# Kernel optimization log

Measured on AMD Instinct MI355X. Metric: run time of the kernel, lower is better.

## Reference

```python
import jax, jax.numpy as jnp
import numpy as np

NHEAD = 16
NUM_GROUPS = 4
EXPERTS_PER_GROUP = 2
LN_EPS = 1e-5


def _layernorm(x, g, b):
    mu = jnp.mean(x, axis=-1, keepdims=True)
    var = jnp.mean(jnp.square(x - mu), axis=-1, keepdims=True)
    return (x - mu) * jax.lax.rsqrt(var + LN_EPS) * g + b


def _mha(x, wi, bi, wo, bo):
    # torch nn.MultiheadAttention (batch_first): qkv = x @ in_proj_w.T + in_proj_b
    B, S, D = x.shape
    hd = D // NHEAD
    qkv = x @ wi.T + bi                      # [B,S,3D]
    q, k, v = jnp.split(qkv, 3, axis=-1)
    def heads(t):
        return t.reshape(B, S, NHEAD, hd).transpose(0, 2, 1, 3)  # [B,H,S,hd]
    q, k, v = heads(q), heads(k), heads(v)
    scores = jnp.einsum('bhqd,bhkd->bhqk', q, k) / jnp.sqrt(jnp.asarray(hd, x.dtype))
    attn = jax.nn.softmax(scores, axis=-1)
    o = jnp.einsum('bhqk,bhkd->bhqd', attn, v)
    o = o.transpose(0, 2, 1, 3).reshape(B, S, D)
    return o @ wo.T + bo


def _hier_moe(x, w_group, b_group, w_expert, b_expert, w1, b1, w2, b2):
    # Two-level top-1 routing: group gate -> expert gate within chosen group.
    B, S, D = x.shape
    xt = x.reshape(B * S, D)                 # [T,D]
    T = xt.shape[0]
    E = NUM_GROUPS * EXPERTS_PER_GROUP

    gp = jax.nn.softmax(xt @ w_group + b_group, axis=-1)          # [T,G]
    g_idx = jnp.argmax(gp, axis=-1)                                # [T]
    g_prob = jnp.max(gp, axis=-1)                                  # [T]

    elog = jnp.einsum('td,gde->tge', xt, w_expert) + b_expert      # [T,G,Epg]
    ep = jax.nn.softmax(elog, axis=-1)
    ep_sel = jnp.take_along_axis(ep, g_idx[:, None, None], axis=1)[:, 0, :]  # [T,Epg]
    e_idx_local = jnp.argmax(ep_sel, axis=-1)                      # [T]
    e_prob = jnp.max(ep_sel, axis=-1)                              # [T]

    flat_e = g_idx * EXPERTS_PER_GROUP + e_idx_local               # [T]
    combine = jax.nn.one_hot(flat_e, E, dtype=xt.dtype) * (g_prob * e_prob)[:, None]  # [T,E]

    # Dense dispatch (reference): run every expert on all tokens, combine with one-hot weights.
    h = jax.nn.relu(jnp.einsum('td,edf->etf', xt, w1) + b1[:, None, :])   # [E,T,Fff]
    y = jnp.einsum('etf,efd->etd', h, w2) + b2[:, None, :]                # [E,T,D]
    out = jnp.einsum('te,etd->td', combine, y)                            # [T,D]
    return out.reshape(B, S, D)


def setup_inputs() -> dict:
    key = jax.random.key(0)
    ks = jax.random.split(key, 8)
    B, S, D, F = 2, 1024, 1024, 2048
    G, Epg = NUM_GROUPS, EXPERTS_PER_GROUP
    E = G * Epg
    sc = lambda fan: 1.0 / np.sqrt(fan)
    return {
        'x': jax.random.normal(ks[0], (B, S, D), jnp.float32),
        'in_proj_w': jax.random.normal(ks[1], (3 * D, D), jnp.float32) * sc(D),
        'in_proj_b': jnp.zeros((3 * D,), jnp.float32),
        'out_proj_w': jax.random.normal(ks[2], (D, D), jnp.float32) * sc(D),
        'out_proj_b': jnp.zeros((D,), jnp.float32),
        'ln1_g': jnp.ones((D,), jnp.float32),
        'ln1_b': jnp.zeros((D,), jnp.float32),
        'ln2_g': jnp.ones((D,), jnp.float32),
        'ln2_b': jnp.zeros((D,), jnp.float32),
        'w_group': jax.random.normal(ks[3], (D, G), jnp.float32) * sc(D),
        'b_group': jnp.zeros((G,), jnp.float32),
        'w_expert': jax.random.normal(ks[4], (G, D, Epg), jnp.float32) * sc(D),
        'b_expert': jnp.zeros((G, Epg), jnp.float32),
        'w1': jax.random.normal(ks[5], (E, D, F), jnp.float32) * sc(D),
        'b1': jnp.zeros((E, F), jnp.float32),
        'w2': jax.random.normal(ks[6], (E, F, D), jnp.float32) * sc(F),
        'b2': jnp.zeros((E, D), jnp.float32),
    }


def reference(x, in_proj_w, in_proj_b, out_proj_w, out_proj_b,
              ln1_g, ln1_b, ln2_g, ln2_b,
              w_group, b_group, w_expert, b_expert, w1, b1, w2, b2):
    # Dropout p=0.1 is identity in eval mode.
    attn_out = _mha(x, in_proj_w, in_proj_b, out_proj_w, out_proj_b)
    x = _layernorm(x + attn_out, ln1_g, ln1_b)
    moe_out = _hier_moe(x, w_group, b_group, w_expert, b_expert, w1, b1, w2, b2)
    x = _layernorm(x + moe_out, ln2_g, ln2_b)
    return x
```

## Files before the change

kernel.cpp:

```cpp
#include <hip/hip_runtime.h>
#include <hip/hip_bf16.h>

#define TT 2048
#define DD 1024
#define FF 2048
#define SS 1024
#define NHD 16
#define HDD 64
#define NG 4
#define EPG 2
#define NE 8

#define QSC 0.18033688011112042f

typedef __attribute__((ext_vector_type(8))) short bf16x8;
typedef __attribute__((ext_vector_type(4))) float f32x4;
typedef __attribute__((ext_vector_type(4))) unsigned short ush4;

__device__ __forceinline__ unsigned short f2bf(float x) {
    unsigned int u = __float_as_uint(x);
    u = (u + 0x7fffu + ((u >> 16) & 1u)) >> 16;
    return (unsigned short)u;
}
__device__ __forceinline__ float bf2f(unsigned short h) {
    return __uint_as_float((unsigned int)h << 16);
}

__device__ __forceinline__ float wave_sum(float s) {
#pragma unroll
    for (int off = 32; off > 0; off >>= 1) s += __shfl_xor(s, off);
    return s;
}

__device__ __forceinline__ void gl16(const void* g, void* l) {
    auto gp = reinterpret_cast<const unsigned int __attribute__((address_space(1)))*>(
        (unsigned long long)g);
    auto lp = reinterpret_cast<unsigned int __attribute__((address_space(3)))*>(
        (unsigned int)(unsigned long long)l);
    __builtin_amdgcn_global_load_lds(gp, lp, 16, 0, 0);
}

__global__ __launch_bounds__(256) void split_bf16_kernel(
    const float* __restrict__ in, unsigned short* __restrict__ hi,
    unsigned short* __restrict__ lo, int n4)
{
    const int i = blockIdx.x * 256 + threadIdx.x;
    if (i >= n4) return;
    const float4 v = ((const float4*)in)[i];
    float vv[4] = {v.x, v.y, v.z, v.w};
    ush4 h, l;
#pragma unroll
    for (int j = 0; j < 4; ++j) {
        const unsigned short hb = f2bf(vv[j]);
        ((unsigned short*)&h)[j] = hb;
        ((unsigned short*)&l)[j] = f2bf(vv[j] - bf2f(hb));
    }
    ((ush4*)hi)[i] = h;
    ((ush4*)lo)[i] = l;
}

__global__ __launch_bounds__(256, 3) void gemm_split_kernel(
    const unsigned short* __restrict__ Ah, const unsigned short* __restrict__ Al,
    const unsigned short* __restrict__ Bh, const unsigned short* __restrict__ Bl,
    const float* __restrict__ bias, const float* __restrict__ resid,
    float* __restrict__ C, unsigned short* __restrict__ Chi,
    unsigned short* __restrict__ Clo, int qscale_n, int M, int N, int K)
{
    __shared__ unsigned short sAh[128 * 64];
    __shared__ unsigned short sAl[128 * 64];
    __shared__ unsigned short sBh[64 * 64];
    __shared__ unsigned short sBl[64 * 64];
    const int tid = threadIdx.x;
    const int lane = tid & 63, wid = tid >> 6;
    const int l15 = lane & 15, lg = lane >> 4;
    const int n0 = blockIdx.x << 6, m0 = blockIdx.y << 7;
    const int kper = K / gridDim.z;
    const int kbeg = blockIdx.z * kper, kend = kbeg + kper;
    float* __restrict__ Cz = C ? (C + (size_t)blockIdx.z * M * N) : C;

    f32x4 acc[2][4];
#pragma unroll
    for (int mi = 0; mi < 2; ++mi)
#pragma unroll
        for (int ni = 0; ni < 4; ++ni) acc[mi][ni] = (f32x4){0.f, 0.f, 0.f, 0.f};

    for (int k0 = kbeg; k0 < kend; k0 += 64) {
#pragma unroll
        for (int r = 0; r < 4; ++r) {
            const int s = (r << 8) + tid;
            const int row = s >> 3;
            const int cs = (s & 7) ^ (row & 7);
            const int lb = (s & ~63) << 3;
            const size_t ga = (size_t)(m0 + row) * K + k0 + (cs << 3);
            gl16(Ah + ga, &sAh[lb]);
            gl16(Al + ga, &sAl[lb]);
        }
#pragma unroll
        for (int r = 0; r < 2; ++r) {
            const int s = (r << 8) + tid;
            const int row = s >> 3;
            const int cs = (s & 7) ^ (row & 7);
            const int lb = (s & ~63) << 3;
            const size_t gb = (size_t)(n0 + row) * K + k0 + (cs << 3);
            gl16(Bh + gb, &sBh[lb]);
            gl16(Bl + gb, &sBl[lb]);
        }
        __syncthreads();
#pragma unroll
        for (int ks = 0; ks < 2; ++ks) {
            bf16x8 ah[2], al[2], bh[4], bl[4];
            const int ac = (ks << 2) + lg;
#pragma unroll
            for (int i = 0; i < 2; ++i) {
                const int ar = (wid << 5) + (i << 4) + l15;
                const int pa = ((ar << 3) | (ac ^ (ar & 7))) << 3;
                ah[i] = *(const bf16x8*)&sAh[pa];
                al[i] = *(const bf16x8*)&sAl[pa];
            }
#pragma unroll
            for (int i = 0; i < 4; ++i) {
                const int br = (i << 4) + l15;
                const int pb = ((br << 3) | (ac ^ (br & 7))) << 3;
                bh[i] = *(const bf16x8*)&sBh[pb];
                bl[i] = *(const bf16x8*)&sBl[pb];
            }
#pragma unroll
            for (int mi = 0; mi < 2; ++mi)
#pragma unroll
                for (int ni = 0; ni < 4; ++ni) {
                    acc[mi][ni] = __builtin_amdgcn_mfma_f32_16x16x32_bf16(ah[mi], bh[ni], acc[mi][ni], 0, 0, 0);
                    acc[mi][ni] = __builtin_amdgcn_mfma_f32_16x16x32_bf16(ah[mi], bl[ni], acc[mi][ni], 0, 0, 0);
                    acc[mi][ni] = __builtin_amdgcn_mfma_f32_16x16x32_bf16(al[mi], bh[ni], acc[mi][ni], 0, 0, 0);
                }
        }
        __syncthreads();
    }
#pragma unroll
    for (int mi = 0; mi < 2; ++mi)
#pragma unroll
        for (int ni = 0; ni < 4; ++ni)
#pragma unroll
            for (int r2 = 0; r2 < 4; ++r2) {
                const int m = m0 + (wid << 5) + (mi << 4) + (lg << 2) + r2;
                const int n = n0 + (ni << 4) + l15;
                float v = acc[mi][ni][r2];
                if (bias) v += bias[n];
                if (resid) v += resid[(size_t)m * N + n];
                const size_t idx = (size_t)m * N + n;
                if (Chi) {
                    if (n < qscale_n) v *= QSC;
                    const unsigned short hb = f2bf(v);
                    Chi[idx] = hb;
                    Clo[idx] = f2bf(v - bf2f(hb));
                } else {
                    Cz[idx] = v;
                }
            }
}

__global__ __launch_bounds__(256) void vtrans_kernel(
    const unsigned short* __restrict__ src, unsigned short* __restrict__ dst)
{
    __shared__ unsigned short tile[64][65];
    const int bh = blockIdx.y, b = bh >> 4, h = bh & 15;
    const int s0 = blockIdx.x << 6;
    const int tid = threadIdx.x;
#pragma unroll
    for (int r = 0; r < 2; ++r) {
        const int sl = tid + (r << 8);
        const int rr = sl >> 3, c8 = (sl & 7) << 3;
        const bf16x8 v = *(const bf16x8*)(src + (size_t)(b * SS + s0 + rr) * 3072 + 2048 + h * HDD + c8);
#pragma unroll
        for (int j = 0; j < 8; ++j) tile[rr][c8 + j] = ((const unsigned short*)&v)[j];
    }
    __syncthreads();
#pragma unroll
    for (int r = 0; r < 2; ++r) {
        const int sl = tid + (r << 8);
        const int d = sl >> 3, s8 = (sl & 7) << 3;
        bf16x8 o;
#pragma unroll
        for (int j = 0; j < 8; ++j) ((unsigned short*)&o)[j] = tile[s8 + j][d];
        *(bf16x8*)(dst + (size_t)(bh * HDD + d) * SS + s0 + s8) = o;
    }
}

__global__ __launch_bounds__(256, 4) void attn_mfma_kernel(
    const unsigned short* __restrict__ qh, const unsigned short* __restrict__ ql,
    const unsigned short* __restrict__ vth, const unsigned short* __restrict__ vtl,
    float* __restrict__ opart, float* __restrict__ mpart, float* __restrict__ lpart)
{
    __shared__ unsigned short sKh[4096], sKl[4096];
    __shared__ unsigned short sVh[4096], sVl[4096];
    const int bh = blockIdx.y, b = bh >> 4, h = bh & 15;
    const int q0 = blockIdx.x << 6;
    const int z = blockIdx.z;
    const int tid = threadIdx.x, lane = tid & 63, w = tid >> 6;
    const int l15 = lane & 15, lg = lane >> 4;

#pragma unroll
    for (int r = 0; r < 2; ++r) {
        const int s = (r << 8) + tid;
        const int row = s >> 3;
        const int cs = (s & 7) ^ (row & 7);
        const int lb = (s & ~63) << 3;
        const size_t gq = (size_t)(b * SS + q0 + row) * 3072 + h * HDD + (cs << 3);
        gl16(qh + gq, &sKh[lb]);
        gl16(ql + gq, &sKl[lb]);
    }
    __syncthreads();
    bf16x8 qah[2], qal[2];
#pragma unroll
    for (int ks = 0; ks < 2; ++ks) {
        const int ar = (w << 4) + l15;
        const int ac = (ks << 2) + lg;
        const int pa = ((ar << 3) | (ac ^ (ar & 7))) << 3;
        qah[ks] = *(const bf16x8*)&sKh[pa];
        qal[ks] = *(const bf16x8*)&sKl[pa];
    }
    __syncthreads();

    f32x4 accO[4];
#pragma unroll
    for (int nt = 0; nt < 4; ++nt) accO[nt] = (f32x4){0.f, 0.f, 0.f, 0.f};
    float m_run = -3.0e38f, l_run = 0.f;

    const int kvbeg = z << 9;
    for (int kv0 = kvbeg; kv0 < kvbeg + 512; kv0 += 64) {
#pragma unroll
        for (int r = 0; r < 2; ++r) {
            const int s = (r << 8) + tid;
            const int row = s >> 3;
            const int cs = (s & 7) ^ (row & 7);
            const int lb = (s & ~63) << 3;
            const size_t gk = (size_t)(b * SS + kv0 + row) * 3072 + DD + h * HDD + (cs << 3);
            gl16(qh + gk, &sKh[lb]);
            gl16(ql + gk, &sKl[lb]);
            const size_t gv = (size_t)(bh * HDD + row) * SS + kv0 + (cs << 3);
            gl16(vth + gv, &sVh[lb]);
            gl16(vtl + gv, &sVl[lb]);
        }
        __syncthreads();

        f32x4 sacc[4];
#pragma unroll
        for (int i = 0; i < 4; ++i) sacc[i] = (f32x4){0.f, 0.f, 0.f, 0.f};
        __builtin_amdgcn_s_setprio(1);
#pragma unroll
        for (int ks = 0; ks < 2; ++ks) {
            const int ac = (ks << 2) + lg;
#pragma unroll
            for (int i = 0; i < 4; ++i) {
                const int br = (i << 4) + l15;
                const int pb = ((br << 3) | (ac ^ (br & 7))) << 3;
                const bf16x8 kbh = *(const bf16x8*)&sKh[pb];
                const bf16x8 kbl = *(const bf16x8*)&sKl[pb];
                sacc[i] = __builtin_amdgcn_mfma_f32_16x16x32_bf16(kbh, qah[ks], sacc[i], 0, 0, 0);
                sacc[i] = __builtin_amdgcn_mfma_f32_16x16x32_bf16(kbh, qal[ks], sacc[i], 0, 0, 0);
                sacc[i] = __builtin_amdgcn_mfma_f32_16x16x32_bf16(kbl, qah[ks], sacc[i], 0, 0, 0);
            }
        }
        __builtin_amdgcn_s_setprio(0);
        __syncthreads();

        float mx = sacc[0][0];
#pragma unroll
        for (int i = 0; i < 4; ++i)
#pragma unroll
            for (int r2 = 0; r2 < 4; ++r2) mx = fmaxf(mx, sacc[i][r2]);
        mx = fmaxf(mx, __shfl_xor(mx, 16));
        mx = fmaxf(mx, __shfl_xor(mx, 32));
        const float mn = fmaxf(m_run, mx);
        const float corr = exp2f(m_run - mn);
        m_run = mn;
        float ls = 0.f;
        const int qrow = (w << 4) | l15;
#pragma unroll
        for (int i = 0; i < 4; ++i) {
            ush4 hp, lp;
#pragma unroll
            for (int r2 = 0; r2 < 4; ++r2) {
                const float p = exp2f(sacc[i][r2] - mn);
                ls += p;
                const unsigned short hb = (unsigned short)(__float_as_uint(p) >> 16);
                hp[r2] = hb;
                lp[r2] = (unsigned short)(__float_as_uint(p - bf2f(hb)) >> 16);
            }
            const int kvb = (i << 4) + (lg << 2);
            const int idx = (qrow << 6) + (((kvb >> 3) ^ (qrow & 7)) << 3) + (kvb & 7);
            *(ush4*)&sKh[idx] = hp;
            *(ush4*)&sKl[idx] = lp;
        }
        ls += __shfl_xor(ls, 16);
        ls += __shfl_xor(ls, 32);
        l_run = l_run * corr + ls;
        float c4[4];
#pragma unroll
        for (int r2 = 0; r2 < 4; ++r2)
            c4[r2] = __shfl(corr, (lane & 48) | ((lg << 2) + r2));
#pragma unroll
        for (int nt = 0; nt < 4; ++nt)
#pragma unroll
            for (int r2 = 0; r2 < 4; ++r2) accO[nt][r2] *= c4[r2];

        __builtin_amdgcn_s_setprio(1);
#pragma unroll
        for (int ks = 0; ks < 2; ++ks) {
            const int qq = (w << 4) + l15;
            const int slot = (ks << 2) + lg;
            const int pidx = (qq << 6) + ((slot ^ (qq & 7)) << 3);
            const bf16x8 pah = *(const bf16x8*)&sKh[pidx];
            const bf16x8 pal = *(const bf16x8*)&sKl[pidx];
            const int ac = (ks << 2) + lg;
#pragma unroll
            for (int nt = 0; nt < 4; ++nt) {
                const int dr = (nt << 4) + l15;
                const int pv = ((dr << 3) | (ac ^ (dr & 7))) << 3;
                const bf16x8 vbh = *(const bf16x8*)&sVh[pv];
                const bf16x8 vbl = *(const bf16x8*)&sVl[pv];
                accO[nt] = __builtin_amdgcn_mfma_f32_16x16x32_bf16(pah, vbh, accO[nt], 0, 0, 0);
                accO[nt] = __builtin_amdgcn_mfma_f32_16x16x32_bf16(pah, vbl, accO[nt], 0, 0, 0);
                accO[nt] = __builtin_amdgcn_mfma_f32_16x16x32_bf16(pal, vbh, accO[nt], 0, 0, 0);
            }
        }
        __builtin_amdgcn_s_setprio(0);
        __syncthreads();
    }

#pragma unroll
    for (int nt = 0; nt < 4; ++nt)
#pragma unroll
        for (int r2 = 0; r2 < 4; ++r2) {
            const int qq = q0 + (w << 4) + (lg << 2) + r2;
            const int dd = h * HDD + (nt << 4) + l15;
            opart[((size_t)z * TT + b * SS + qq) * DD + dd] = accO[nt][r2];
        }
    if (lane < 16) {
        const int qq = q0 + (w << 4) + lane;
        const int idx = z * (32 * SS) + bh * SS + qq;
        mpart[idx] = m_run;
        lpart[idx] = l_run;
    }
}

__global__ __launch_bounds__(256) void attn_combine_kernel(
    const float* __restrict__ opart, const float* __restrict__ mpart,
    const float* __restrict__ lpart, unsigned short* __restrict__ ohi,
    unsigned short* __restrict__ olo)
{
    const int t = blockIdx.x;
    const int tid = threadIdx.x;
    const int b = t >> 10, q = t & 1023;
    const int d0 = tid << 2;
    const int bh = (b << 4) + (d0 >> 6);
    const int mi = bh * SS + q;
    const float m0 = mpart[mi], m1 = mpart[32 * SS + mi];
    const float l0 = lpart[mi], l1 = lpart[32 * SS + mi];
    const float m = fmaxf(m0, m1);
    const float e0 = exp2f(m0 - m), e1 = exp2f(m1 - m);
    const float inv = 1.0f / (l0 * e0 + l1 * e1);
    const float4 a = *(const float4*)(opart + (size_t)t * DD + d0);
    const float4 c = *(const float4*)(opart + (size_t)(TT + t) * DD + d0);
    const float vv[4] = { (a.x * e0 + c.x * e1) * inv, (a.y * e0 + c.y * e1) * inv,
                          (a.z * e0 + c.z * e1) * inv, (a.w * e0 + c.w * e1) * inv };
    ush4 hh, ll;
#pragma unroll
    for (int j = 0; j < 4; ++j) {
        const unsigned short hb = f2bf(vv[j]);
        hh[j] = hb;
        ll[j] = f2bf(vv[j] - bf2f(hb));
    }
    *(ush4*)(ohi + (size_t)t * DD + d0) = hh;
    *(ush4*)(olo + (size_t)t * DD + d0) = ll;
}

__global__ __launch_bounds__(256) void ln_kernel(
    const float* __restrict__ in, const float* __restrict__ gamma,
    const float* __restrict__ beta, float* __restrict__ outf)
{
    const int t = blockIdx.x;
    const int tid = threadIdx.x;
    __shared__ float red[8];
    const float4 v = ((const float4*)(in + (size_t)t * DD))[tid];
    float s = v.x + v.y + v.z + v.w;
    s = wave_sum(s);
    const int wid = tid >> 6, lane = tid & 63;
    if (lane == 0) red[wid] = s;
    __syncthreads();
    const float mu = (red[0] + red[1] + red[2] + red[3]) * (1.0f / DD);
    const float d0 = v.x - mu, d1 = v.y - mu, d2 = v.z - mu, d3 = v.w - mu;
    float q = d0 * d0 + d1 * d1 + d2 * d2 + d3 * d3;
    q = wave_sum(q);
    if (lane == 0) red[4 + wid] = q;
    __syncthreads();
    const float var = (red[4] + red[5] + red[6] + red[7]) * (1.0f / DD);
    const float rstd = 1.0f / sqrtf(var + 1e-5f);
    const float4 g4 = ((const float4*)gamma)[tid];
    const float4 b4 = ((const float4*)beta)[tid];
    float4 ov = { d0 * rstd * g4.x + b4.x, d1 * rstd * g4.y + b4.y,
                  d2 * rstd * g4.z + b4.z, d3 * rstd * g4.w + b4.w };
    ((float4*)(outf + (size_t)t * DD))[tid] = ov;
}

__global__ __launch_bounds__(256) void ln_route_kernel(
    const float* __restrict__ x, const float* __restrict__ p0,
    const float* __restrict__ p1, const float* __restrict__ bo,
    const float* __restrict__ gamma, const float* __restrict__ beta,
    float* __restrict__ outf, unsigned short* __restrict__ outb,
    const float* __restrict__ wg, const float* __restrict__ bg,
    const float* __restrict__ we, const float* __restrict__ be,
    int* __restrict__ eid, float* __restrict__ gate, int* __restrict__ counts)
{
    const int t = blockIdx.x;
    const int tid = threadIdx.x;
    __shared__ float red[8];
    __shared__ float red2[4][12];
    const float4 xv = ((const float4*)(x + (size_t)t * DD))[tid];
    const float4 a4 = ((const float4*)(p0 + (size_t)t * DD))[tid];
    const float4 c4v = ((const float4*)(p1 + (size_t)t * DD))[tid];
    const float4 bo4 = ((const float4*)bo)[tid];
    const float4 v = { xv.x + a4.x + c4v.x + bo4.x, xv.y + a4.y + c4v.y + bo4.y,
                       xv.z + a4.z + c4v.z + bo4.z, xv.w + a4.w + c4v.w + bo4.w };
    float s = v.x + v.y + v.z + v.w;
    s = wave_sum(s);
    const int wid = tid >> 6, lane = tid & 63;
    if (lane == 0) red[wid] = s;
    __syncthreads();
    const float mu = (red[0] + red[1] + red[2] + red[3]) * (1.0f / DD);
    const float d0 = v.x - mu, d1 = v.y - mu, d2 = v.z - mu, d3 = v.w - mu;
    float q = d0 * d0 + d1 * d1 + d2 * d2 + d3 * d3;
    q = wave_sum(q);
    if (lane == 0) red[4 + wid] = q;
    __syncthreads();
    const float var = (red[4] + red[5] + red[6] + red[7]) * (1.0f / DD);
    const float rstd = 1.0f / sqrtf(var + 1e-5f);
    const float4 g4 = ((const float4*)gamma)[tid];
    const float4 b4 = ((const float4*)beta)[tid];
    const float o0 = d0 * rstd * g4.x + b4.x;
    const float o1 = d1 * rstd * g4.y + b4.y;
    const float o2 = d2 * rstd * g4.z + b4.z;
    const float o3 = d3 * rstd * g4.w + b4.w;
    float4 ov = {o0, o1, o2, o3};
    ((float4*)(outf + (size_t)t * DD))[tid] = ov;
    ush4 wv = { f2bf(o0), f2bf(o1), f2bf(o2), f2bf(o3) };
    *(ush4*)(outb + (size_t)t * DD + (tid << 2)) = wv;

    float pz[12];
#pragma unroll
    for (int k = 0; k < 12; ++k) pz[k] = 0.f;
    const float xo[4] = {o0, o1, o2, o3};
#pragma unroll
    for (int j = 0; j < 4; ++j) {
        const int c = (tid << 2) + j;
        const float xvv = xo[j];
        const float4 wgv = *(const float4*)(wg + c * NG);
        pz[0] = fmaf(xvv, wgv.x, pz[0]);
        pz[1] = fmaf(xvv, wgv.y, pz[1]);
        pz[2] = fmaf(xvv, wgv.z, pz[2]);
        pz[3] = fmaf(xvv, wgv.w, pz[3]);
#pragma unroll
        for (int g = 0; g < NG; ++g) {
            const float2 wev = *(const float2*)(we + ((size_t)g * DD + c) * EPG);
            pz[4 + 2 * g]     = fmaf(xvv, wev.x, pz[4 + 2 * g]);
            pz[4 + 2 * g + 1] = fmaf(xvv, wev.y, pz[4 + 2 * g + 1]);
        }
    }
#pragma unroll
    for (int k = 0; k < 12; ++k) pz[k] = wave_sum(pz[k]);
    if (lane == 0) {
#pragma unroll
        for (int k = 0; k < 12; ++k) red2[wid][k] = pz[k];
    }
    __syncthreads();
    if (tid == 0) {
        float zs[12];
#pragma unroll
        for (int k = 0; k < 12; ++k)
            zs[k] = red2[0][k] + red2[1][k] + red2[2][k] + red2[3][k];
        float z[NG];
#pragma unroll
        for (int g = 0; g < NG; ++g) z[g] = zs[g] + bg[g];
        int gi = 0; float zb = z[0];
#pragma unroll
        for (int g = 1; g < NG; ++g) if (z[g] > zb) { zb = z[g]; gi = g; }
        float se = 0.f;
#pragma unroll
        for (int g = 0; g < NG; ++g) se += __expf(z[g] - zb);
        const float gprob = 1.0f / se;
        float e0 = 0.f, e1 = 0.f;
#pragma unroll
        for (int g = 0; g < NG; ++g) {
            if (g == gi) {
                e0 = zs[4 + 2 * g] + be[g * EPG + 0];
                e1 = zs[4 + 2 * g + 1] + be[g * EPG + 1];
            }
        }
        const int ei = (e1 > e0) ? 1 : 0;
        const float ehi = ei ? e1 : e0, elo = ei ? e0 : e1;
        const float eprob = 1.0f / (1.0f + __expf(elo - ehi));
        eid[t] = gi * EPG + ei;
        gate[t] = gprob * eprob;
        atomicAdd(&counts[gi * EPG + ei], 1);
    }
}

__global__ void zero_counts_kernel(int* __restrict__ counts) {
    if (threadIdx.x < NE) counts[threadIdx.x] = 0;
}

__global__ void offsets_kernel(const int* __restrict__ counts, int* __restrict__ offs,
                               int* __restrict__ cursor) {
    if (threadIdx.x == 0) {
        int run = 0;
        for (int e = 0; e < NE; ++e) { offs[e] = run; cursor[e] = run; run += counts[e]; }
        offs[NE] = run;
    }
}

__global__ __launch_bounds__(256) void scatter_kernel(const int* __restrict__ eid,
                                                      int* __restrict__ cursor,
                                                      int* __restrict__ perm) {
    const int t = blockIdx.x * 256 + threadIdx.x;
    const int slot = atomicAdd(&cursor[eid[t]], 1);
    perm[slot] = t;
}

__global__ __launch_bounds__(256) void transpose_bf16_kernel(
    const float* __restrict__ in, unsigned short* __restrict__ out, int R, int C)
{
    __shared__ float tile[32][33];
    const int c0 = blockIdx.x << 5, r0 = blockIdx.y << 5;
    const size_t bo = (size_t)blockIdx.z * R * C;
    const int tc = threadIdx.x & 31, tr8 = threadIdx.x >> 5;
#pragma unroll
    for (int p = 0; p < 4; ++p) {
        const int rr = tr8 + (p << 3);
        tile[rr][tc] = in[bo + (size_t)(r0 + rr) * C + c0 + tc];
    }
    __syncthreads();
#pragma unroll
    for (int p = 0; p < 4; ++p) {
        const int rr = tr8 + (p << 3);
        out[bo + (size_t)(c0 + rr) * R + r0 + tc] = f2bf(tile[tc][rr]);
    }
}

__global__ __launch_bounds__(256, 4) void moe_gemm1_kernel(
    const unsigned short* __restrict__ x1b, const unsigned short* __restrict__ w1t,
    const float* __restrict__ b1, const int* __restrict__ offs,
    const int* __restrict__ perm, unsigned short* __restrict__ hbuf)
{
    const int e = blockIdx.y >> 5, mt = blockIdx.y & 31;
    const int row0 = offs[e] + (mt << 6);
    const int rend = offs[e + 1];
    if (row0 >= rend) return;
    const int valid = min(rend - row0, 64);
    const int n0 = blockIdx.x << 6;
    __shared__ unsigned short sA[2][64 * 64];
    __shared__ unsigned short sB[2][64 * 64];
    const int tid = threadIdx.x;
    const int lane = tid & 63, w = tid >> 6;
    const int l15 = lane & 15, lg = lane >> 4;

    size_t abase[2], bbase[2];
    int lbs[2];
#pragma unroll
    for (int r = 0; r < 2; ++r) {
        const int s = (r << 8) + tid;
        const int row = s >> 3;
        const int cs = (s & 7) ^ (row & 7);
        lbs[r] = (s & ~63) << 3;
        const int tk = perm[min(row0 + row, rend - 1)];
        abase[r] = (size_t)tk * DD + (cs << 3);
        bbase[r] = ((size_t)e * FF + n0 + row) * DD + (cs << 3);
    }

    f32x4 acc[4];
#pragma unroll
    for (int nt = 0; nt < 4; ++nt) acc[nt] = (f32x4){0.f, 0.f, 0.f, 0.f};

#pragma unroll
    for (int r = 0; r < 2; ++r) {
        gl16(x1b + abase[r], &sA[0][lbs[r]]);
        gl16(w1t + bbase[r], &sB[0][lbs[r]]);
    }
    __syncthreads();
    int cur = 0;
    for (int k0 = 0; k0 < DD; k0 += 64) {
        const int nxt = k0 + 64;
        if (nxt < DD) {
#pragma unroll
            for (int r = 0; r < 2; ++r) {
                gl16(x1b + abase[r] + nxt, &sA[cur ^ 1][lbs[r]]);
                gl16(w1t + bbase[r] + nxt, &sB[cur ^ 1][lbs[r]]);
            }
        }
#pragma unroll
        for (int ks = 0; ks < 2; ++ks) {
            const int ac = (ks << 2) + lg;
            const int ar = (w << 4) + l15;
            const int pa = ((ar << 3) | (ac ^ (ar & 7))) << 3;
            const bf16x8 a = *(const bf16x8*)&sA[cur][pa];
#pragma unroll
            for (int nt = 0; nt < 4; ++nt) {
                const int br = (nt << 4) + l15;
                const int pb = ((br << 3) | (ac ^ (br & 7))) << 3;
                acc[nt] = __builtin_amdgcn_mfma_f32_16x16x32_bf16(
                    a, *(const bf16x8*)&sB[cur][pb], acc[nt], 0, 0, 0);
            }
        }
        __syncthreads();
        cur ^= 1;
    }

    const float* bias = b1 + e * FF + n0;
    const int mbase = (w << 4) + (lg << 2);
#pragma unroll
    for (int nt = 0; nt < 4; ++nt) {
        const int n = (nt << 4) + l15;
#pragma unroll
        for (int r2 = 0; r2 < 4; ++r2) {
            const int m = mbase + r2;
            if (m < valid) {
                float v = fmaxf(acc[nt][r2] + bias[n], 0.f);
                hbuf[(size_t)(row0 + m) * FF + n0 + n] = f2bf(v);
            }
        }
    }
}

__global__ __launch_bounds__(256, 4) void moe_gemm2_kernel(
    const unsigned short* __restrict__ hbuf, const unsigned short* __restrict__ w2t,
    const int* __restrict__ offs, float* __restrict__ p0, float* __restrict__ p1)
{
    const int e = blockIdx.y >> 5, mt = blockIdx.y & 31;
    const int row0 = offs[e] + (mt << 6);
    const int rend = offs[e + 1];
    if (row0 >= rend) return;
    const int valid = min(rend - row0, 64);
    const int n0 = blockIdx.x << 6;
    const int z = blockIdx.z;
    float* __restrict__ pbuf = z ? p1 : p0;
    __shared__ unsigned short sA[2][64 * 64];
    __shared__ unsigned short sB[2][64 * 64];
    const int tid = threadIdx.x;
    const int lane = tid & 63, w = tid >> 6;
    const int l15 = lane & 15, lg = lane >> 4;

    size_t abase[2], bbase[2];
    int lbs[2];
#pragma unroll
    for (int r = 0; r < 2; ++r) {
        const int s = (r << 8) + tid;
        const int row = s >> 3;
        const int cs = (s & 7) ^ (row & 7);
        lbs[r] = (s & ~63) << 3;
        abase[r] = (size_t)(row0 + row) * FF + (cs << 3);
        bbase[r] = ((size_t)e * DD + n0 + row) * FF + (cs << 3);
    }

    f32x4 acc[4];
#pragma unroll
    for (int nt = 0; nt < 4; ++nt) acc[nt] = (f32x4){0.f, 0.f, 0.f, 0.f};

    const int kbeg = z << 10, kend = kbeg + 1024;
#pragma unroll
    for (int r = 0; r < 2; ++r) {
        gl16(hbuf + abase[r] + kbeg, &sA[0][lbs[r]]);
        gl16(w2t + bbase[r] + kbeg, &sB[0][lbs[r]]);
    }
    __syncthreads();
    int cur = 0;
    for (int k0 = kbeg; k0 < kend; k0 += 64) {
        const int nxt = k0 + 64;
        if (nxt < kend) {
#pragma unroll
            for (int r = 0; r < 2; ++r) {
                gl16(hbuf + abase[r] + nxt, &sA[cur ^ 1][lbs[r]]);
                gl16(w2t + bbase[r] + nxt, &sB[cur ^ 1][lbs[r]]);
            }
        }
#pragma unroll
        for (int ks = 0; ks < 2; ++ks) {
            const int ac = (ks << 2) + lg;
            const int ar = (w << 4) + l15;
            const int pa = ((ar << 3) | (ac ^ (ar & 7))) << 3;
            const bf16x8 a = *(const bf16x8*)&sA[cur][pa];
#pragma unroll
            for (int nt = 0; nt < 4; ++nt) {
                const int br = (nt << 4) + l15;
                const int pb = ((br << 3) | (ac ^ (br & 7))) << 3;
                acc[nt] = __builtin_amdgcn_mfma_f32_16x16x32_bf16(
                    a, *(const bf16x8*)&sB[cur][pb], acc[nt], 0, 0, 0);
            }
        }
        __syncthreads();
        cur ^= 1;
    }

    const int mbase = (w << 4) + (lg << 2);
#pragma unroll
    for (int nt = 0; nt < 4; ++nt) {
        const int n = (nt << 4) + l15;
#pragma unroll
        for (int r2 = 0; r2 < 4; ++r2) {
            const int m = mbase + r2;
            if (m < valid) pbuf[(size_t)(row0 + m) * DD + n0 + n] = acc[nt][r2];
        }
    }
}

__global__ __launch_bounds__(256) void moe2_combine_kernel(
    const float* __restrict__ p0, const float* __restrict__ p1,
    const int* __restrict__ offs, const int* __restrict__ perm,
    const float* __restrict__ gate, const float* __restrict__ b2,
    const float* __restrict__ x1, float* __restrict__ res2)
{
    const int s = blockIdx.x;
    const int tid = threadIdx.x;
    int e = 0;
#pragma unroll
    for (int g = 1; g < NE; ++g) e += (s >= offs[g]) ? 1 : 0;
    const int tk = perm[s];
    const float gt = gate[tk];
    const int c0 = tid << 2;
    const float4 a  = *(const float4*)(p0 + (size_t)s * DD + c0);
    const float4 b  = *(const float4*)(p1 + (size_t)s * DD + c0);
    const float4 bb = *(const float4*)(b2 + (size_t)e * DD + c0);
    const float4 xx = *(const float4*)(x1 + (size_t)tk * DD + c0);
    float4 o = { xx.x + gt * (a.x + b.x + bb.x), xx.y + gt * (a.y + b.y + bb.y),
                 xx.z + gt * (a.z + b.z + bb.z), xx.w + gt * (a.w + b.w + bb.w) };
    *(float4*)(res2 + (size_t)tk * DD + c0) = o;
}

extern "C" void kernel_launch(void* const* d_in, const int* in_sizes, int n_in,
                              void* d_out, int out_size, void* d_ws, size_t ws_size,
                              hipStream_t stream)
{
    (void)in_sizes; (void)n_in; (void)out_size; (void)ws_size;
    const float* x   = (const float*)d_in[0];
    const float* wi  = (const float*)d_in[1];
    const float* bi  = (const float*)d_in[2];
    const float* wo  = (const float*)d_in[3];
    const float* bo  = (const float*)d_in[4];
    const float* g1  = (const float*)d_in[5];
    const float* be1 = (const float*)d_in[6];
    const float* g2  = (const float*)d_in[7];
    const float* be2 = (const float*)d_in[8];
    const float* wgr = (const float*)d_in[9];
    const float* bgr = (const float*)d_in[10];
    const float* wex = (const float*)d_in[11];
    const float* bex = (const float*)d_in[12];
    const float* w1  = (const float*)d_in[13];
    const float* b1  = (const float*)d_in[14];
    const float* w2  = (const float*)d_in[15];
    const float* b2  = (const float*)d_in[16];
    float* out = (float*)d_out;

    char* ws = (char*)d_ws;
    unsigned short* qkvh  = (unsigned short*)(ws + 0);
    unsigned short* qkvl  = (unsigned short*)(ws + 12582912);
    unsigned short* hbuf  = (unsigned short*)(ws + 0);
    float* res2           = (float*)(ws + 8388608);
    unsigned short* vth   = (unsigned short*)(ws + 25165824);
    unsigned short* vtl   = (unsigned short*)(ws + 29360128);
    float* x1             = (float*)(ws + 41943040);
    unsigned short* x1b   = (unsigned short*)(ws + 50331648);
    unsigned short* w1t   = (unsigned short*)(ws + 54525952);
    unsigned short* w2t   = (unsigned short*)(ws + 88080384);
    char* misc = ws + 121634816;
    int*   eid    = (int*)(misc);
    float* gate   = (float*)(misc + 8192);
    int*   perm   = (int*)(misc + 16384);
    int*   counts = (int*)(misc + 24576);
    int*   offs   = (int*)(misc + 24640);
    int*   cursor = (int*)(misc + 24704);

    unsigned short* xs_hi = (unsigned short*)(ws + 33554432);
    unsigned short* xs_lo = (unsigned short*)(ws + 33554432 + 4194304);
    unsigned short* wi_hi = (unsigned short*)(ws + 54525952);
    unsigned short* wi_lo = (unsigned short*)(ws + 54525952 + 6291456);
    unsigned short* o_hi  = (unsigned short*)(ws + 41943040);
    unsigned short* o_lo  = (unsigned short*)(ws + 41943040 + 4194304);
    unsigned short* wo_hi = (unsigned short*)(ws + 88080384);
    unsigned short* wo_lo = (unsigned short*)(ws + 88080384 + 2097152);

    float* opart = (float*)(ws + 54525952);
    float* mpart = (float*)(ws + 54525952 + 16777216);
    float* lpart = (float*)(ws + 54525952 + 17039360);

    float* oproj = (float*)(ws + 0);

    float* mp0 = (float*)(ws + 16777216);
    float* mp1 = (float*)(ws + 25165824);

    zero_counts_kernel<<<dim3(1), dim3(64), 0, stream>>>(counts);

    split_bf16_kernel<<<dim3((TT * DD / 4 + 255) / 256), dim3(256), 0, stream>>>(x, xs_hi, xs_lo, TT * DD / 4);
    split_bf16_kernel<<<dim3((3 * DD * DD / 4 + 255) / 256), dim3(256), 0, stream>>>(wi, wi_hi, wi_lo, 3 * DD * DD / 4);
    gemm_split_kernel<<<dim3(3 * DD / 64, TT / 128, 1), dim3(256), 0, stream>>>(
        xs_hi, xs_lo, wi_hi, wi_lo, bi, (const float*)nullptr,
        (float*)nullptr, qkvh, qkvl, DD, TT, 3 * DD, DD);

    vtrans_kernel<<<dim3(SS / 64, 2 * NHD), dim3(256), 0, stream>>>(qkvh, vth);
    vtrans_kernel<<<dim3(SS / 64, 2 * NHD), dim3(256), 0, stream>>>(qkvl, vtl);

    attn_mfma_kernel<<<dim3(SS / 64, 2 * NHD, 2), dim3(256), 0, stream>>>(
        qkvh, qkvl, vth, vtl, opart, mpart, lpart);
    attn_combine_kernel<<<dim3(TT), dim3(256), 0, stream>>>(opart, mpart, lpart, o_hi, o_lo);

    split_bf16_kernel<<<dim3((DD * DD / 4 + 255) / 256), dim3(256), 0, stream>>>(wo, wo_hi, wo_lo, DD * DD / 4);
    gemm_split_kernel<<<dim3(DD / 64, TT / 128, 2), dim3(256), 0, stream>>>(
        o_hi, o_lo, wo_hi, wo_lo, (const float*)nullptr, (const float*)nullptr,
        oproj, (unsigned short*)nullptr, (unsigned short*)nullptr, 0, TT, DD, DD);

    ln_route_kernel<<<dim3(TT), dim3(256), 0, stream>>>(
        x, oproj, oproj + (size_t)TT * DD, bo, g1, be1, x1, x1b,
        wgr, bgr, wex, bex, eid, gate, counts);
    offsets_kernel<<<dim3(1), dim3(64), 0, stream>>>(counts, offs, cursor);
    scatter_kernel<<<dim3(TT / 256), dim3(256), 0, stream>>>(eid, cursor, perm);

    transpose_bf16_kernel<<<dim3(FF / 32, DD / 32, NE), dim3(256), 0, stream>>>(w1, w1t, DD, FF);
    transpose_bf16_kernel<<<dim3(DD / 32, FF / 32, NE), dim3(256), 0, stream>>>(w2, w2t, FF, DD);

    moe_gemm1_kernel<<<dim3(FF / 64, NE * 32), dim3(256), 0, stream>>>(x1b, w1t, b1, offs, perm, hbuf);
    moe_gemm2_kernel<<<dim3(DD / 64, NE * 32, 2), dim3(256), 0, stream>>>(hbuf, w2t, offs, mp0, mp1);
    moe2_combine_kernel<<<dim3(TT), dim3(256), 0, stream>>>(mp0, mp1, offs, perm, gate, b2, x1, res2);

    ln_kernel<<<dim3(TT), dim3(256), 0, stream>>>(res2, g2, be2, out);
}
```

Baseline: 273.7 us.

## Double-buffer split-bf16 GEMM with interleaved hi/lo tiles; merge small launches

The split-precision GEMM now keeps hi and lo halves of each 32-wide K chunk interleaved in a single swizzled shared tile. It double-buffers these tiles so the next chunk's global-to-LDS copy is issued before the current chunk's MFMAs, with one barrier per iteration instead of two. Separately, the two V-transpose launches are merged into one grid using a z dimension, and the offsets and scatter kernels are fused into a single-block kernel using shared-memory atomics. The aim is to hide load latency and cut launch overhead, at the cost of a shorter K step per iteration and a serial single-block scatter.

```diff
diff --git a/kernel.cpp b/kernel.cpp
--- a/kernel.cpp
+++ b/kernel.cpp
@@ -66,10 +66,8 @@
     float* __restrict__ C, unsigned short* __restrict__ Chi,
     unsigned short* __restrict__ Clo, int qscale_n, int M, int N, int K)
 {
-    __shared__ unsigned short sAh[128 * 64];
-    __shared__ unsigned short sAl[128 * 64];
-    __shared__ unsigned short sBh[64 * 64];
-    __shared__ unsigned short sBl[64 * 64];
+    __shared__ unsigned short sA[2][128 * 64];
+    __shared__ unsigned short sB[2][64 * 64];
     const int tid = threadIdx.x;
     const int lane = tid & 63, wid = tid >> 6;
     const int l15 = lane & 15, lg = lane >> 4;
@@ -78,62 +76,76 @@
     const int kbeg = blockIdx.z * kper, kend = kbeg + kper;
     float* __restrict__ Cz = C ? (C + (size_t)blockIdx.z * M * N) : C;
 
+    const unsigned short* aplane[4];
+    size_t asrc[4];
+    int albs[4];
+#pragma unroll
+    for (int r = 0; r < 4; ++r) {
+        const int s = (r << 8) + tid;
+        const int row = s >> 3, p = s & 7;
+        const int c = p ^ (row & 7);
+        aplane[r] = (c < 4) ? Ah : Al;
+        asrc[r] = (size_t)(m0 + row) * K + ((c & 3) << 3);
+        albs[r] = (s & ~63) << 3;
+    }
+    const unsigned short* bplane[2];
+    size_t bsrc[2];
+    int blbs[2];
+#pragma unroll
+    for (int r = 0; r < 2; ++r) {
+        const int s = (r << 8) + tid;
+        const int row = s >> 3, p = s & 7;
+        const int c = p ^ (row & 7);
+        bplane[r] = (c < 4) ? Bh : Bl;
+        bsrc[r] = (size_t)(n0 + row) * K + ((c & 3) << 3);
+        blbs[r] = (s & ~63) << 3;
+    }
+
+    auto stage = [&](int buf, int k0) {
+#pragma unroll
+        for (int r = 0; r < 4; ++r) gl16(aplane[r] + asrc[r] + k0, &sA[buf][albs[r]]);
+#pragma unroll
+        for (int r = 0; r < 2; ++r) gl16(bplane[r] + bsrc[r] + k0, &sB[buf][blbs[r]]);
+    };
+
     f32x4 acc[2][4];
 #pragma unroll
     for (int mi = 0; mi < 2; ++mi)
 #pragma unroll
         for (int ni = 0; ni < 4; ++ni) acc[mi][ni] = (f32x4){0.f, 0.f, 0.f, 0.f};
 
-    for (int k0 = kbeg; k0 < kend; k0 += 64) {
-#pragma unroll
-        for (int r = 0; r < 4; ++r) {
-            const int s = (r << 8) + tid;
-            const int row = s >> 3;
-            const int cs = (s & 7) ^ (row & 7);
-            const int lb = (s & ~63) << 3;
-            const size_t ga = (size_t)(m0 + row) * K + k0 + (cs << 3);
-            gl16(Ah + ga, &sAh[lb]);
-            gl16(Al + ga, &sAl[lb]);
-        }
-#pragma unroll
-        for (int r = 0; r < 2; ++r) {
-            const int s = (r << 8) + tid;
-            const int row = s >> 3;
-            const int cs = (s & 7) ^ (row & 7);
-            const int lb = (s & ~63) << 3;
-            const size_t gb = (size_t)(n0 + row) * K + k0 + (cs << 3);
-            gl16(Bh + gb, &sBh[lb]);
-            gl16(Bl + gb, &sBl[lb]);
-        }
+    stage(0, kbeg);
+    __syncthreads();
+    int cur = 0;
+    for (int k0 = kbeg; k0 < kend; k0 += 32) {
+        if (k0 + 32 < kend) stage(cur ^ 1, k0 + 32);
+        bf16x8 ah[2], al[2], bh[4], bl[4];
+#pragma unroll
+        for (int mi = 0; mi < 2; ++mi) {
+            const int ar = (wid << 5) + (mi << 4) + l15;
+            const int ph = lg ^ (ar & 7);
+            const int base = ar << 6;
+            ah[mi] = *(const bf16x8*)&sA[cur][base + (ph << 3)];
+            al[mi] = *(const bf16x8*)&sA[cur][base + ((ph ^ 4) << 3)];
+        }
+#pragma unroll
+        for (int ni = 0; ni < 4; ++ni) {
+            const int br = (ni << 4) + l15;
+            const int ph = lg ^ (br & 7);
+            const int base = br << 6;
+            bh[ni] = *(const bf16x8*)&sB[cur][base + (ph << 3)];
+            bl[ni] = *(const bf16x8*)&sB[cur][base + ((ph ^ 4) << 3)];
+        }
+#pragma unroll
+        for (int mi = 0; mi < 2; ++mi)
+#pragma unroll
+            for (int ni = 0; ni < 4; ++ni) {
+                acc[mi][ni] = __builtin_amdgcn_mfma_f32_16x16x32_bf16(ah[mi], bh[ni], acc[mi][ni], 0, 0, 0);
+                acc[mi][ni] = __builtin_amdgcn_mfma_f32_16x16x32_bf16(ah[mi], bl[ni], acc[mi][ni], 0, 0, 0);
+                acc[mi][ni] = __builtin_amdgcn_mfma_f32_16x16x32_bf16(al[mi], bh[ni], acc[mi][ni], 0, 0, 0);
+            }
         __syncthreads();
-#pragma unroll
-        for (int ks = 0; ks < 2; ++ks) {
-            bf16x8 ah[2], al[2], bh[4], bl[4];
-            const int ac = (ks << 2) + lg;
-#pragma unroll
-            for (int i = 0; i < 2; ++i) {
-                const int ar = (wid << 5) + (i << 4) + l15;
-                const int pa = ((ar << 3) | (ac ^ (ar & 7))) << 3;
-                ah[i] = *(const bf16x8*)&sAh[pa];
-                al[i] = *(const bf16x8*)&sAl[pa];
-            }
-#pragma unroll
-            for (int i = 0; i < 4; ++i) {
-                const int br = (i << 4) + l15;
-                const int pb = ((br << 3) | (ac ^ (br & 7))) << 3;
-                bh[i] = *(const bf16x8*)&sBh[pb];
-                bl[i] = *(const bf16x8*)&sBl[pb];
-            }
-#pragma unroll
-            for (int mi = 0; mi < 2; ++mi)
-#pragma unroll
-                for (int ni = 0; ni < 4; ++ni) {
-                    acc[mi][ni] = __builtin_amdgcn_mfma_f32_16x16x32_bf16(ah[mi], bh[ni], acc[mi][ni], 0, 0, 0);
-                    acc[mi][ni] = __builtin_amdgcn_mfma_f32_16x16x32_bf16(ah[mi], bl[ni], acc[mi][ni], 0, 0, 0);
-                    acc[mi][ni] = __builtin_amdgcn_mfma_f32_16x16x32_bf16(al[mi], bh[ni], acc[mi][ni], 0, 0, 0);
-                }
-        }
-        __syncthreads();
+        cur ^= 1;
     }
 #pragma unroll
     for (int mi = 0; mi < 2; ++mi)
@@ -159,9 +171,12 @@
 }
 
 __global__ __launch_bounds__(256) void vtrans_kernel(
-    const unsigned short* __restrict__ src, unsigned short* __restrict__ dst)
+    const unsigned short* __restrict__ srch, const unsigned short* __restrict__ srcl,
+    unsigned short* __restrict__ dsth, unsigned short* __restrict__ dstl)
 {
     __shared__ unsigned short tile[64][65];
+    const unsigned short* __restrict__ src = blockIdx.z ? srcl : srch;
+    unsigned short* __restrict__ dst = blockIdx.z ? dstl : dsth;
     const int bh = blockIdx.y, b = bh >> 4, h = bh & 15;
     const int s0 = blockIdx.x << 6;
     const int tid = threadIdx.x;
@@ -508,21 +523,23 @@
     if (threadIdx.x < NE) counts[threadIdx.x] = 0;
 }
 
-__global__ void offsets_kernel(const int* __restrict__ counts, int* __restrict__ offs,
-                               int* __restrict__ cursor) {
+__global__ __launch_bounds__(256) void route_scatter_kernel(
+    const int* __restrict__ eid, const int* __restrict__ counts,
+    int* __restrict__ offs, int* __restrict__ perm)
+{
+    __shared__ int loff[NE + 1];
+    __shared__ int lcur[NE];
     if (threadIdx.x == 0) {
         int run = 0;
-        for (int e = 0; e < NE; ++e) { offs[e] = run; cursor[e] = run; run += counts[e]; }
-        offs[NE] = run;
-    }
-}
-
-__global__ __launch_bounds__(256) void scatter_kernel(const int* __restrict__ eid,
-                                                      int* __restrict__ cursor,
-                                                      int* __restrict__ perm) {
-    const int t = blockIdx.x * 256 + threadIdx.x;
-    const int slot = atomicAdd(&cursor[eid[t]], 1);
-    perm[slot] = t;
+        for (int e = 0; e < NE; ++e) { loff[e] = run; lcur[e] = run; run += counts[e]; }
+        loff[NE] = run;
+    }
+    __syncthreads();
+    for (int t = threadIdx.x; t < TT; t += 256) {
+        const int slot = atomicAdd(&lcur[eid[t]], 1);
+        perm[slot] = t;
+    }
+    if (threadIdx.x <= NE) offs[threadIdx.x] = loff[threadIdx.x];
 }
 
 __global__ __launch_bounds__(256) void transpose_bf16_kernel(
@@ -774,7 +791,6 @@
     int*   perm   = (int*)(misc + 16384);
     int*   counts = (int*)(misc + 24576);
     int*   offs   = (int*)(misc + 24640);
-    int*   cursor = (int*)(misc + 24704);
 
     unsigned short* xs_hi = (unsigned short*)(ws + 33554432);
     unsigned short* xs_lo = (unsigned short*)(ws + 33554432 + 4194304);
@@ -802,8 +818,7 @@
         xs_hi, xs_lo, wi_hi, wi_lo, bi, (const float*)nullptr,
         (float*)nullptr, qkvh, qkvl, DD, TT, 3 * DD, DD);
 
-    vtrans_kernel<<<dim3(SS / 64, 2 * NHD), dim3(256), 0, stream>>>(qkvh, vth);
-    vtrans_kernel<<<dim3(SS / 64, 2 * NHD), dim3(256), 0, stream>>>(qkvl, vtl);
+    vtrans_kernel<<<dim3(SS / 64, 2 * NHD, 2), dim3(256), 0, stream>>>(qkvh, qkvl, vth, vtl);
 
     attn_mfma_kernel<<<dim3(SS / 64, 2 * NHD, 2), dim3(256), 0, stream>>>(
         qkvh, qkvl, vth, vtl, opart, mpart, lpart);
@@ -817,8 +832,7 @@
     ln_route_kernel<<<dim3(TT), dim3(256), 0, stream>>>(
         x, oproj, oproj + (size_t)TT * DD, bo, g1, be1, x1, x1b,
         wgr, bgr, wex, bex, eid, gate, counts);
-    offsets_kernel<<<dim3(1), dim3(64), 0, stream>>>(counts, offs, cursor);
-    scatter_kernel<<<dim3(TT / 256), dim3(256), 0, stream>>>(eid, cursor, perm);
+    route_scatter_kernel<<<dim3(1), dim3(256), 0, stream>>>(eid, counts, offs, perm);
 
     transpose_bf16_kernel<<<dim3(FF / 32, DD / 32, NE), dim3(256), 0, stream>>>(w1, w1t, DD, FF);
     transpose_bf16_kernel<<<dim3(DD / 32, FF / 32, NE), dim3(256), 0, stream>>>(w2, w2t, FF, DD);
```

New measurement: 276.8 us. No clear change (+1.1%).
